# Performance work log

Hardware: AMD Instinct MI355X
Metric: run time of the kernel (lower is better)

The kernel has to match this reference:

```python
import jax, jax.numpy as jnp
import numpy as np

N_NODES = 50000
N_EDGES = 800000
IN_FEATS = 128
H_FEATS = 128
OUT_FEATS = 64
N_HEADS = 4
THRESHOLD = 0.1
COS_EPS = 1e-8   # F.cosine_similarity eps
LN_EPS = 1e-5


def setup_inputs() -> dict:
    key = jax.random.key(0)
    ks = jax.random.split(key, 16)
    D1 = H_FEATS // N_HEADS  # 32
    inp = {
        "feat": jax.random.normal(ks[0], (N_NODES, IN_FEATS), dtype=jnp.float32),
        "src": jax.random.randint(ks[1], (N_EDGES,), 0, N_NODES, dtype=jnp.int32),
        "dst": jax.random.randint(ks[2], (N_EDGES,), 0, N_NODES, dtype=jnp.int32),
        # conv0: in_feats -> n_heads * (h_feats // n_heads)
        "W0": jax.random.normal(ks[3], (IN_FEATS, N_HEADS * D1), dtype=jnp.float32) * (1.0 / np.sqrt(IN_FEATS)),
        "b0": jnp.zeros((N_HEADS * D1,), dtype=jnp.float32),
        # conv1: h_feats -> n_heads * (h_feats // n_heads)
        "W1": jax.random.normal(ks[4], (H_FEATS, N_HEADS * D1), dtype=jnp.float32) * (1.0 / np.sqrt(H_FEATS)),
        "b1": jnp.zeros((N_HEADS * D1,), dtype=jnp.float32),
        # conv2: h_feats -> 1 * out_feats
        "W2": jax.random.normal(ks[5], (H_FEATS, OUT_FEATS), dtype=jnp.float32) * (1.0 / np.sqrt(H_FEATS)),
        "b2": jnp.zeros((OUT_FEATS,), dtype=jnp.float32),
        # LayerNorms used after conv0 and conv1 (lns[1], lns[2])
        "ln1_g": jnp.ones((H_FEATS,), dtype=jnp.float32),
        "ln1_b": jnp.zeros((H_FEATS,), dtype=jnp.float32),
        "ln2_g": jnp.ones((H_FEATS,), dtype=jnp.float32),
        "ln2_b": jnp.zeros((H_FEATS,), dtype=jnp.float32),
    }
    return inp


def _layer_norm(x, g, b):
    mu = jnp.mean(x, axis=-1, keepdims=True)
    var = jnp.mean(jnp.square(x - mu), axis=-1, keepdims=True)
    return (x - mu) * jax.lax.rsqrt(var + LN_EPS) * g + b


def _rgat_conv(x, src, dst, W, b, n_heads, d_out):
    N = x.shape[0]
    ft = (x @ W).reshape(N, n_heads, d_out)  # (N, H, D)
    # edge score: cosine_similarity(src_feat_flat, src_feat_flat) -> per-node, then gather
    flat = ft.reshape(N, n_heads * d_out)
    sq = jnp.sum(flat * flat, axis=1)                      # (N,)
    nrm = jnp.maximum(jnp.sqrt(sq), COS_EPS)
    cos = sq / (nrm * nrm)                                 # ~1 for nonzero rows
    e_node = jnp.log(jnp.where(cos >= THRESHOLD, cos, 1e-6))
    e = e_node[src]                                        # (E,)
    # segment softmax over destination nodes (DGL edge_softmax)
    m = jax.ops.segment_max(e, dst, num_segments=N)
    m = jnp.where(jnp.isfinite(m), m, 0.0)                 # empty segments
    ex = jnp.exp(e - m[dst])
    den = jax.ops.segment_sum(ex, dst, num_segments=N)
    a = ex / jnp.maximum(den[dst], 1e-16)                  # (E,)
    # u_mul_e + sum aggregation
    msg = ft[src] * a[:, None, None]                       # (E, H, D)
    out = jax.ops.segment_sum(msg, dst, num_segments=N)    # (N, H, D)
    return out + b.reshape(1, n_heads, d_out)


def reference(feat, src, dst, W0, b0, W1, b1, W2, b2, ln1_g, ln1_b, ln2_g, ln2_b):
    N = feat.shape[0]
    D1 = H_FEATS // N_HEADS
    x = _rgat_conv(feat, src, dst, W0, b0, N_HEADS, D1).reshape(N, -1)
    x = jax.nn.relu(_layer_norm(x, ln1_g, ln1_b))
    x = _rgat_conv(x, src, dst, W1, b1, N_HEADS, D1).reshape(N, -1)
    x = jax.nn.relu(_layer_norm(x, ln2_g, ln2_b))
    x = _rgat_conv(x, src, dst, W2, b2, 1, OUT_FEATS).reshape(N, -1)
    return x
```

## Files before the change

kernel.cpp:

```cpp
#include <hip/hip_runtime.h>
#include <hip/hip_fp16.h>
#include <math.h>

#define NN 50000
#define NE 800000
#define NB 196
#define CPAD 16
#define STILE 4096
#define BCAP 8192

typedef _Float16 v8h __attribute__((ext_vector_type(8)));
typedef float v4f __attribute__((ext_vector_type(4)));

__global__ __launch_bounds__(256) void convert_kernel(
    const float* __restrict__ W0, const float* __restrict__ W1,
    const float* __restrict__ W2, __half* __restrict__ W0T,
    __half* __restrict__ W1T, __half* __restrict__ W2T,
    int* __restrict__ bhist) {
  int gid = blockIdx.x * 256 + threadIdx.x;
  if (gid < NB * CPAD) bhist[gid] = 0;
  if (gid < 16384) {
    int n = gid >> 7, k = gid & 127;
    W0T[gid] = __float2half(W0[k * 128 + n]);
  } else if (gid < 32768) {
    int g = gid - 16384; int n = g >> 7, k = g & 127;
    W1T[g] = __float2half(W1[k * 128 + n]);
  } else if (gid < 40960) {
    int g = gid - 32768; int n = g >> 7, k = g & 127;
    W2T[g] = __float2half(W2[k * 64 + n]);
  }
}

template <int OUT, bool F32IN>
__global__ __launch_bounds__(256) void gemm_mfma(
    const void* __restrict__ Xv, const __half* __restrict__ WT,
    __half* __restrict__ Y, int nrows) {
  constexpr int NT = OUT / 16;
  __shared__ __align__(16) __half Xs[64][136];
  __shared__ __align__(16) __half Ws[OUT][136];
  const int tid = threadIdx.x;
  const int row0 = blockIdx.x * 64;
#pragma unroll
  for (int i = 0; i < 4; i++) {
    int ci = tid + 256 * i;
    int r = ci >> 4, ch = ci & 15;
    int g = row0 + r;
    if (F32IN) {
      const float* X32 = (const float*)Xv;
      float4 a0 = make_float4(0.f, 0.f, 0.f, 0.f), a1 = a0;
      if (g < nrows) {
        a0 = *(const float4*)&X32[(size_t)g * 128 + ch * 8];
        a1 = *(const float4*)&X32[(size_t)g * 128 + ch * 8 + 4];
      }
      union { __half2 h2[4]; int4 i4; } u;
      u.h2[0] = __floats2half2_rn(a0.x, a0.y);
      u.h2[1] = __floats2half2_rn(a0.z, a0.w);
      u.h2[2] = __floats2half2_rn(a1.x, a1.y);
      u.h2[3] = __floats2half2_rn(a1.z, a1.w);
      *(int4*)&Xs[r][ch * 8] = u.i4;
    } else {
      const __half* X16 = (const __half*)Xv;
      int4 v = make_int4(0, 0, 0, 0);
      if (g < nrows) v = *(const int4*)&X16[(size_t)g * 128 + ch * 8];
      *(int4*)&Xs[r][ch * 8] = v;
    }
  }
#pragma unroll
  for (int i = 0; i < NT; i++) {
    int ci = tid + 256 * i;
    int n = ci >> 4, ch = ci & 15;
    *(int4*)&Ws[n][ch * 8] = *(const int4*)&WT[(size_t)n * 128 + ch * 8];
  }
  __syncthreads();
  const int lane = tid & 63;
  const int w = tid >> 6;
  const int c16 = lane & 15, q = lane >> 4;
  v8h a[4];
#pragma unroll
  for (int kt = 0; kt < 4; kt++)
    a[kt] = *(const v8h*)&Xs[w * 16 + c16][kt * 32 + q * 8];
  v4f acc[NT];
#pragma unroll
  for (int t = 0; t < NT; t++) acc[t] = (v4f){0.f, 0.f, 0.f, 0.f};
#pragma unroll
  for (int t = 0; t < NT; t++) {
#pragma unroll
    for (int kt = 0; kt < 4; kt++) {
      v8h bfr = *(const v8h*)&Ws[t * 16 + c16][kt * 32 + q * 8];
      acc[t] = __builtin_amdgcn_mfma_f32_16x16x32_f16(a[kt], bfr, acc[t], 0, 0, 0);
    }
  }
#pragma unroll
  for (int t = 0; t < NT; t++)
#pragma unroll
    for (int r = 0; r < 4; r++)
      Xs[w * 16 + q * 4 + r][t * 16 + c16] = __float2half(acc[t][r]);
  __syncthreads();
  constexpr int OCH = OUT / 8;
#pragma unroll
  for (int i = 0; i < 64 * OCH / 256; i++) {
    int ci = tid + 256 * i;
    int r = ci / OCH, ch = ci % OCH;
    int g = row0 + r;
    if (g < nrows) *(int4*)&Y[(size_t)g * OUT + ch * 8] = *(const int4*)&Xs[r][ch * 8];
  }
}

template <int F, bool LN, bool HOUT>
__global__ __launch_bounds__(256) void agg_kernel(
    const __half* __restrict__ ft,
    const int* __restrict__ row_ptr, const unsigned short* __restrict__ es,
    const float* __restrict__ bias, const float* __restrict__ g,
    const float* __restrict__ beta, void* __restrict__ out_v, int n) {
  int gw = (blockIdx.x * blockDim.x + threadIdx.x) >> 6;
  int lane = threadIdx.x & 63;
  if (gw >= n) return;
  int b = row_ptr[gw], e = row_ptr[gw + 1];
  int deg = e - b;

  constexpr int LPR = F / 8;
  constexpr int EW  = 64 / LPR;
  const int sub = lane / LPR;
  const int ll  = lane % LPR;
  __half2 hacc[4];
#pragma unroll
  for (int q = 0; q < 4; q++) hacc[q] = __floats2half2_rn(0.f, 0.f);

  for (int cb = b; cb < e; cb += 64) {
    int rem = e - cb; if (rem > 64) rem = 64;
    int sn_l = 0;
    if (lane < rem) sn_l = es[cb + lane];
    for (int j = 0; j < rem; j += EW) {
      int jj = j + sub;
      int sn = __shfl(sn_l, jj, 64);
      if (jj < rem) {
        union { float4 f4; __half2 h2[4]; } u;
        u.f4 = *(const float4*)&ft[(size_t)sn * F + ll * 8];
#pragma unroll
        for (int q = 0; q < 4; q++) hacc[q] = __hadd2(hacc[q], u.h2[q]);
      }
    }
  }

#pragma unroll
  for (int o = 32; o >= LPR; o >>= 1) {
#pragma unroll
    for (int q = 0; q < 4; q++) {
      union { __half2 h; int i; } a, s;
      a.h = hacc[q];
      s.i = __shfl_xor(a.i, o, 64);
      hacc[q] = __hadd2(a.h, s.h);
    }
  }

  float acc[8];
#pragma unroll
  for (int q = 0; q < 4; q++) {
    float2 f = __half22float2(hacc[q]);
    acc[2 * q + 0] = f.x;
    acc[2 * q + 1] = f.y;
  }

  float sc = (deg > 0) ? (1.0f / (float)deg) : 0.f;
  float4 b4a = *(const float4*)&bias[ll * 8 + 0];
  float4 b4b = *(const float4*)&bias[ll * 8 + 4];
  acc[0] = fmaf(acc[0], sc, b4a.x); acc[1] = fmaf(acc[1], sc, b4a.y);
  acc[2] = fmaf(acc[2], sc, b4a.z); acc[3] = fmaf(acc[3], sc, b4a.w);
  acc[4] = fmaf(acc[4], sc, b4b.x); acc[5] = fmaf(acc[5], sc, b4b.y);
  acc[6] = fmaf(acc[6], sc, b4b.z); acc[7] = fmaf(acc[7], sc, b4b.w);

  if (LN) {
    float sum = 0.f;
#pragma unroll
    for (int q = 0; q < 8; q++) sum += acc[q];
#pragma unroll
    for (int o = LPR / 2; o > 0; o >>= 1) sum += __shfl_xor(sum, o, 64);
    float mean = sum * (1.0f / 128.0f);
    float var = 0.f;
#pragma unroll
    for (int q = 0; q < 8; q++) { acc[q] -= mean; var = fmaf(acc[q], acc[q], var); }
#pragma unroll
    for (int o = LPR / 2; o > 0; o >>= 1) var += __shfl_xor(var, o, 64);
    float r = rsqrtf(var * (1.0f / 128.0f) + 1e-5f);
    float4 g4a = *(const float4*)&g[ll * 8 + 0];
    float4 g4b = *(const float4*)&g[ll * 8 + 4];
    float4 be4a = *(const float4*)&beta[ll * 8 + 0];
    float4 be4b = *(const float4*)&beta[ll * 8 + 4];
    acc[0] = fmaxf(acc[0] * r * g4a.x + be4a.x, 0.f);
    acc[1] = fmaxf(acc[1] * r * g4a.y + be4a.y, 0.f);
    acc[2] = fmaxf(acc[2] * r * g4a.z + be4a.z, 0.f);
    acc[3] = fmaxf(acc[3] * r * g4a.w + be4a.w, 0.f);
    acc[4] = fmaxf(acc[4] * r * g4b.x + be4b.x, 0.f);
    acc[5] = fmaxf(acc[5] * r * g4b.y + be4b.y, 0.f);
    acc[6] = fmaxf(acc[6] * r * g4b.z + be4b.z, 0.f);
    acc[7] = fmaxf(acc[7] * r * g4b.w + be4b.w, 0.f);
  }
  if (sub == 0) {
    if (HOUT) {
      __half* outh = (__half*)out_v;
      union { __half2 h2[4]; int4 i4; } u;
      u.h2[0] = __floats2half2_rn(acc[0], acc[1]);
      u.h2[1] = __floats2half2_rn(acc[2], acc[3]);
      u.h2[2] = __floats2half2_rn(acc[4], acc[5]);
      u.h2[3] = __floats2half2_rn(acc[6], acc[7]);
      *(int4*)&outh[(size_t)gw * F + ll * 8] = u.i4;
    } else {
      float* outf = (float*)out_v;
      *(float4*)&outf[(size_t)gw * F + ll * 8 + 0] = make_float4(acc[0], acc[1], acc[2], acc[3]);
      *(float4*)&outf[(size_t)gw * F + ll * 8 + 4] = make_float4(acc[4], acc[5], acc[6], acc[7]);
    }
  }
}

__global__ __launch_bounds__(256) void stage_kernel(const int* __restrict__ src,
                                                    const int* __restrict__ dst,
                                                    int* __restrict__ bhist,
                                                    int* __restrict__ staged) {
  __shared__ int cnt[256];
  __shared__ int basep[256];
  __shared__ int cur[256];
  int tid = threadIdx.x;
  cnt[tid] = 0;
  cur[tid] = 0;
  __syncthreads();
#pragma unroll
  for (int q = 0; q < 4; q++) {
    int base = blockIdx.x * STILE + q * 1024 + tid * 4;
    if (base + 3 < NE) {
      int4 d = *(const int4*)&dst[base];
      atomicAdd(&cnt[d.x >> 8], 1);
      atomicAdd(&cnt[d.y >> 8], 1);
      atomicAdd(&cnt[d.z >> 8], 1);
      atomicAdd(&cnt[d.w >> 8], 1);
    } else {
#pragma unroll
      for (int k = 0; k < 4; k++)
        if (base + k < NE) atomicAdd(&cnt[dst[base + k] >> 8], 1);
    }
  }
  __syncthreads();
  if (tid < NB) basep[tid] = (cnt[tid] > 0) ? atomicAdd(&bhist[tid * CPAD], cnt[tid]) : 0;
  __syncthreads();
#pragma unroll
  for (int q = 0; q < 4; q++) {
    int base = blockIdx.x * STILE + q * 1024 + tid * 4;
    if (base + 3 < NE) {
      int4 d = *(const int4*)&dst[base];
      int4 s = *(const int4*)&src[base];
      int b0 = d.x >> 8, b1 = d.y >> 8, b2 = d.z >> 8, b3 = d.w >> 8;
      int p0 = atomicAdd(&cur[b0], 1);
      staged[b0 * BCAP + basep[b0] + p0] = s.x | ((d.x & 255) << 16);
      int p1 = atomicAdd(&cur[b1], 1);
      staged[b1 * BCAP + basep[b1] + p1] = s.y | ((d.y & 255) << 16);
      int p2 = atomicAdd(&cur[b2], 1);
      staged[b2 * BCAP + basep[b2] + p2] = s.z | ((d.z & 255) << 16);
      int p3 = atomicAdd(&cur[b3], 1);
      staged[b3 * BCAP + basep[b3] + p3] = s.w | ((d.w & 255) << 16);
    } else {
#pragma unroll
      for (int k = 0; k < 4; k++) {
        if (base + k < NE) {
          int d = dst[base + k], s = src[base + k];
          int bb = d >> 8;
          int pp = atomicAdd(&cur[bb], 1);
          staged[bb * BCAP + basep[bb] + pp] = s | ((d & 255) << 16);
        }
      }
    }
  }
}

__global__ __launch_bounds__(256) void bucket_csr_kernel(const int* __restrict__ staged,
                                                         const int* __restrict__ bhist,
                                                         int* __restrict__ row_ptr,
                                                         unsigned short* __restrict__ es) {
  int b = blockIdx.x;
  int tid = threadIdx.x;
  int lane = tid & 63, wid = tid >> 6;
  __shared__ int sbase[256];
  __shared__ int wsum[4];
  __shared__ int cnt[256];
  __shared__ int fill_l[256];
  int tv = (tid < NB) ? bhist[tid * CPAD] : 0;
  int x = tv;
#pragma unroll
  for (int o = 1; o < 64; o <<= 1) {
    int y = __shfl_up(x, o, 64);
    if (lane >= o) x += y;
  }
  if (lane == 63) wsum[wid] = x;
  __syncthreads();
  int wpre = 0;
  for (int w = 0; w < wid; w++) wpre += wsum[w];
  sbase[tid] = wpre + x - tv;
  cnt[tid] = 0;
  __syncthreads();
  int lo = sbase[b];
  int cntb = bhist[b * CPAD];
  const int* st = &staged[b * BCAP];
  for (int i = tid; i < cntb; i += 256)
    atomicAdd(&cnt[(st[i] >> 16) & 255], 1);
  __syncthreads();
  int v = cnt[tid];
  x = v;
#pragma unroll
  for (int o = 1; o < 64; o <<= 1) {
    int y = __shfl_up(x, o, 64);
    if (lane >= o) x += y;
  }
  __syncthreads();
  if (lane == 63) wsum[wid] = x;
  __syncthreads();
  wpre = 0;
  for (int w = 0; w < wid; w++) wpre += wsum[w];
  int start = lo + wpre + x - v;
  int node = (b << 8) + tid;
  if (node < NN) row_ptr[node] = start;
  fill_l[tid] = start;
  __syncthreads();
  for (int i = tid; i < cntb; i += 256) {
    int w = st[i];
    int pos = atomicAdd(&fill_l[(w >> 16) & 255], 1);
    es[pos] = (unsigned short)(w & 0xFFFF);
  }
  if (b == 0 && tid == 0) row_ptr[NN] = NE;
}

extern "C" void kernel_launch(void* const* d_in, const int* in_sizes, int n_in,
                              void* d_out, int out_size, void* d_ws, size_t ws_size,
                              hipStream_t stream) {
  (void)in_sizes; (void)n_in; (void)out_size; (void)ws_size;
  const float* feat = (const float*)d_in[0];
  const int* src = (const int*)d_in[1];
  const int* dst = (const int*)d_in[2];
  const float* W0 = (const float*)d_in[3];
  const float* b0 = (const float*)d_in[4];
  const float* W1 = (const float*)d_in[5];
  const float* b1 = (const float*)d_in[6];
  const float* W2 = (const float*)d_in[7];
  const float* b2 = (const float*)d_in[8];
  const float* ln1g = (const float*)d_in[9];
  const float* ln1b = (const float*)d_in[10];
  const float* ln2g = (const float*)d_in[11];
  const float* ln2b = (const float*)d_in[12];
  float* out = (float*)d_out;

  char* p = (char*)d_ws;
  auto alloc = [&](size_t bytes) {
    char* r = p;
    p += (bytes + 255) & ~size_t(255);
    return r;
  };
  __half* fth      = (__half*)alloc((size_t)NN * 128 * 2);
  __half* hh       = (__half*)alloc((size_t)NN * 128 * 2);
  __half* W0T      = (__half*)alloc(128 * 128 * 2);
  __half* W1T      = (__half*)alloc(128 * 128 * 2);
  __half* W2T      = (__half*)alloc(64 * 128 * 2);
  int* row_ptr     = (int*)alloc((size_t)(NN + 1) * 4);
  unsigned short* es = (unsigned short*)alloc((size_t)NE * 2);
  int* staged      = (int*)alloc((size_t)NB * BCAP * 4);
  int* bhist       = (int*)alloc((size_t)NB * CPAD * 4);

  convert_kernel<<<160, 256, 0, stream>>>(W0, W1, W2, W0T, W1T, W2T, bhist);

  int sb = (NE + STILE - 1) / STILE;
  stage_kernel<<<sb, 256, 0, stream>>>(src, dst, bhist, staged);
  bucket_csr_kernel<<<NB, 256, 0, stream>>>(staged, bhist, row_ptr, es);

  int gb = (NN + 63) / 64;
  int nwb = (NN + 3) / 4;

  gemm_mfma<128, true><<<gb, 256, 0, stream>>>(feat, W0T, fth, NN);
  agg_kernel<128, true, true><<<nwb, 256, 0, stream>>>(fth, row_ptr, es, b0, ln1g, ln1b, hh, NN);
  gemm_mfma<128, false><<<gb, 256, 0, stream>>>(hh, W1T, fth, NN);
  agg_kernel<128, true, true><<<nwb, 256, 0, stream>>>(fth, row_ptr, es, b1, ln2g, ln2b, hh, NN);
  gemm_mfma<64, false><<<gb, 256, 0, stream>>>(hh, W2T, fth, NN);
  agg_kernel<64, false, false><<<nwb, 256, 0, stream>>>(fth, row_ptr, es, b2, nullptr, nullptr, out, NN);
}
```

Baseline: 238.9 us.

## Split aggregation into 32-column chunks and move LayerNorm into next GEMM prologue

The aggregation kernel now launches one wave per node per 32-feature column chunk, using blockIdx.y to select the chunk. Each lane loads two neighbor rows per iteration, which gives more waves and more independent loads in flight for the gather. Because a wave no longer sees a whole row, LayerNorm+ReLU moves out of aggregation and into the next GEMM's input-loading stage, using 16-lane shuffles per row. The cost is that each node's edge list is read several times (once per chunk), and the per-row LN statistics are computed on fp16-rounded aggregates.

```diff
diff --git a/kernel.cpp b/kernel.cpp
--- a/kernel.cpp
+++ b/kernel.cpp
@@ -31,9 +31,10 @@
   }
 }
 
-template <int OUT, bool F32IN>
+template <int OUT, bool F32IN, bool LN>
 __global__ __launch_bounds__(256) void gemm_mfma(
     const void* __restrict__ Xv, const __half* __restrict__ WT,
+    const float* __restrict__ lng, const float* __restrict__ lnb,
     __half* __restrict__ Y, int nrows) {
   constexpr int NT = OUT / 16;
   __shared__ __align__(16) __half Xs[64][136];
@@ -62,7 +63,47 @@
       const __half* X16 = (const __half*)Xv;
       int4 v = make_int4(0, 0, 0, 0);
       if (g < nrows) v = *(const int4*)&X16[(size_t)g * 128 + ch * 8];
-      *(int4*)&Xs[r][ch * 8] = v;
+      if (LN) {
+        union { int4 i4; __half2 h2[4]; } u; u.i4 = v;
+        float x[8];
+#pragma unroll
+        for (int q = 0; q < 4; q++) {
+          float2 f = __half22float2(u.h2[q]);
+          x[2 * q + 0] = f.x; x[2 * q + 1] = f.y;
+        }
+        float s = 0.f;
+#pragma unroll
+        for (int q = 0; q < 8; q++) s += x[q];
+#pragma unroll
+        for (int o = 1; o < 16; o <<= 1) s += __shfl_xor(s, o, 64);
+        float mean = s * (1.0f / 128.0f);
+        float var = 0.f;
+#pragma unroll
+        for (int q = 0; q < 8; q++) { x[q] -= mean; var = fmaf(x[q], x[q], var); }
+#pragma unroll
+        for (int o = 1; o < 16; o <<= 1) var += __shfl_xor(var, o, 64);
+        float rr = rsqrtf(var * (1.0f / 128.0f) + 1e-5f);
+        float4 g4a = *(const float4*)&lng[ch * 8 + 0];
+        float4 g4b = *(const float4*)&lng[ch * 8 + 4];
+        float4 bea = *(const float4*)&lnb[ch * 8 + 0];
+        float4 beb = *(const float4*)&lnb[ch * 8 + 4];
+        x[0] = fmaxf(fmaf(x[0] * rr, g4a.x, bea.x), 0.f);
+        x[1] = fmaxf(fmaf(x[1] * rr, g4a.y, bea.y), 0.f);
+        x[2] = fmaxf(fmaf(x[2] * rr, g4a.z, bea.z), 0.f);
+        x[3] = fmaxf(fmaf(x[3] * rr, g4a.w, bea.w), 0.f);
+        x[4] = fmaxf(fmaf(x[4] * rr, g4b.x, beb.x), 0.f);
+        x[5] = fmaxf(fmaf(x[5] * rr, g4b.y, beb.y), 0.f);
+        x[6] = fmaxf(fmaf(x[6] * rr, g4b.z, beb.z), 0.f);
+        x[7] = fmaxf(fmaf(x[7] * rr, g4b.w, beb.w), 0.f);
+        union { __half2 h2[4]; int4 i4; } w;
+        w.h2[0] = __floats2half2_rn(x[0], x[1]);
+        w.h2[1] = __floats2half2_rn(x[2], x[3]);
+        w.h2[2] = __floats2half2_rn(x[4], x[5]);
+        w.h2[3] = __floats2half2_rn(x[6], x[7]);
+        *(int4*)&Xs[r][ch * 8] = w.i4;
+      } else {
+        *(int4*)&Xs[r][ch * 8] = v;
+      }
     }
   }
 #pragma unroll
@@ -106,44 +147,48 @@
   }
 }
 
-template <int F, bool LN, bool HOUT>
-__global__ __launch_bounds__(256) void agg_kernel(
+template <int F, bool F32OUT>
+__global__ __launch_bounds__(256) void agg_chunk_kernel(
     const __half* __restrict__ ft,
     const int* __restrict__ row_ptr, const unsigned short* __restrict__ es,
-    const float* __restrict__ bias, const float* __restrict__ g,
-    const float* __restrict__ beta, void* __restrict__ out_v, int n) {
-  int gw = (blockIdx.x * blockDim.x + threadIdx.x) >> 6;
+    const float* __restrict__ bias, void* __restrict__ out_v, int n) {
+  int gw = blockIdx.x * 4 + (threadIdx.x >> 6);
   int lane = threadIdx.x & 63;
+  int chk = blockIdx.y;
   if (gw >= n) return;
   int b = row_ptr[gw], e = row_ptr[gw + 1];
   int deg = e - b;
 
-  constexpr int LPR = F / 8;
-  constexpr int EW  = 64 / LPR;
-  const int sub = lane / LPR;
-  const int ll  = lane % LPR;
+  const int sub = lane >> 2;
+  const int ll = lane & 3;
+  const __half* ftc = ft + (size_t)chk * 32 + (size_t)ll * 8;
+
   __half2 hacc[4];
 #pragma unroll
   for (int q = 0; q < 4; q++) hacc[q] = __floats2half2_rn(0.f, 0.f);
 
   for (int cb = b; cb < e; cb += 64) {
     int rem = e - cb; if (rem > 64) rem = 64;
-    int sn_l = 0;
-    if (lane < rem) sn_l = es[cb + lane];
-    for (int j = 0; j < rem; j += EW) {
-      int jj = j + sub;
-      int sn = __shfl(sn_l, jj, 64);
-      if (jj < rem) {
-        union { float4 f4; __half2 h2[4]; } u;
-        u.f4 = *(const float4*)&ft[(size_t)sn * F + ll * 8];
-#pragma unroll
-        for (int q = 0; q < 4; q++) hacc[q] = __hadd2(hacc[q], u.h2[q]);
-      }
-    }
-  }
-
-#pragma unroll
-  for (int o = 32; o >= LPR; o >>= 1) {
+    int sn_l = (lane < rem) ? (int)es[cb + lane] : 0;
+    for (int j = 0; j < rem; j += 32) {
+      int jj0 = j + sub;
+      int jj1 = j + 16 + sub;
+      int sn0 = __shfl(sn_l, jj0, 64);
+      int sn1 = __shfl(sn_l, jj1 & 63, 64);
+      union { float4 f4; __half2 h2[4]; } u0, u1;
+      u0.f4 = make_float4(0.f, 0.f, 0.f, 0.f);
+      u1.f4 = make_float4(0.f, 0.f, 0.f, 0.f);
+      if (jj0 < rem) u0.f4 = *(const float4*)&ftc[(size_t)sn0 * F];
+      if (jj1 < rem) u1.f4 = *(const float4*)&ftc[(size_t)sn1 * F];
+#pragma unroll
+      for (int q = 0; q < 4; q++) hacc[q] = __hadd2(hacc[q], u0.h2[q]);
+#pragma unroll
+      for (int q = 0; q < 4; q++) hacc[q] = __hadd2(hacc[q], u1.h2[q]);
+    }
+  }
+
+#pragma unroll
+  for (int o = 32; o >= 4; o >>= 1) {
 #pragma unroll
     for (int q = 0; q < 4; q++) {
       union { __half2 h; int i; } a, s;
@@ -153,61 +198,35 @@
     }
   }
 
-  float acc[8];
-#pragma unroll
-  for (int q = 0; q < 4; q++) {
-    float2 f = __half22float2(hacc[q]);
-    acc[2 * q + 0] = f.x;
-    acc[2 * q + 1] = f.y;
-  }
-
-  float sc = (deg > 0) ? (1.0f / (float)deg) : 0.f;
-  float4 b4a = *(const float4*)&bias[ll * 8 + 0];
-  float4 b4b = *(const float4*)&bias[ll * 8 + 4];
-  acc[0] = fmaf(acc[0], sc, b4a.x); acc[1] = fmaf(acc[1], sc, b4a.y);
-  acc[2] = fmaf(acc[2], sc, b4a.z); acc[3] = fmaf(acc[3], sc, b4a.w);
-  acc[4] = fmaf(acc[4], sc, b4b.x); acc[5] = fmaf(acc[5], sc, b4b.y);
-  acc[6] = fmaf(acc[6], sc, b4b.z); acc[7] = fmaf(acc[7], sc, b4b.w);
-
-  if (LN) {
-    float sum = 0.f;
-#pragma unroll
-    for (int q = 0; q < 8; q++) sum += acc[q];
-#pragma unroll
-    for (int o = LPR / 2; o > 0; o >>= 1) sum += __shfl_xor(sum, o, 64);
-    float mean = sum * (1.0f / 128.0f);
-    float var = 0.f;
-#pragma unroll
-    for (int q = 0; q < 8; q++) { acc[q] -= mean; var = fmaf(acc[q], acc[q], var); }
-#pragma unroll
-    for (int o = LPR / 2; o > 0; o >>= 1) var += __shfl_xor(var, o, 64);
-    float r = rsqrtf(var * (1.0f / 128.0f) + 1e-5f);
-    float4 g4a = *(const float4*)&g[ll * 8 + 0];
-    float4 g4b = *(const float4*)&g[ll * 8 + 4];
-    float4 be4a = *(const float4*)&beta[ll * 8 + 0];
-    float4 be4b = *(const float4*)&beta[ll * 8 + 4];
-    acc[0] = fmaxf(acc[0] * r * g4a.x + be4a.x, 0.f);
-    acc[1] = fmaxf(acc[1] * r * g4a.y + be4a.y, 0.f);
-    acc[2] = fmaxf(acc[2] * r * g4a.z + be4a.z, 0.f);
-    acc[3] = fmaxf(acc[3] * r * g4a.w + be4a.w, 0.f);
-    acc[4] = fmaxf(acc[4] * r * g4b.x + be4b.x, 0.f);
-    acc[5] = fmaxf(acc[5] * r * g4b.y + be4b.y, 0.f);
-    acc[6] = fmaxf(acc[6] * r * g4b.z + be4b.z, 0.f);
-    acc[7] = fmaxf(acc[7] * r * g4b.w + be4b.w, 0.f);
-  }
   if (sub == 0) {
-    if (HOUT) {
+    float acc[8];
+#pragma unroll
+    for (int q = 0; q < 4; q++) {
+      float2 f = __half22float2(hacc[q]);
+      acc[2 * q + 0] = f.x;
+      acc[2 * q + 1] = f.y;
+    }
+    float sc = (deg > 0) ? (1.0f / (float)deg) : 0.f;
+    float4 b4a = *(const float4*)&bias[chk * 32 + ll * 8 + 0];
+    float4 b4b = *(const float4*)&bias[chk * 32 + ll * 8 + 4];
+    acc[0] = fmaf(acc[0], sc, b4a.x); acc[1] = fmaf(acc[1], sc, b4a.y);
+    acc[2] = fmaf(acc[2], sc, b4a.z); acc[3] = fmaf(acc[3], sc, b4a.w);
+    acc[4] = fmaf(acc[4], sc, b4b.x); acc[5] = fmaf(acc[5], sc, b4b.y);
+    acc[6] = fmaf(acc[6], sc, b4b.z); acc[7] = fmaf(acc[7], sc, b4b.w);
+    if (F32OUT) {
+      float* outf = (float*)out_v;
+      *(float4*)&outf[(size_t)gw * F + chk * 32 + ll * 8 + 0] =
+          make_float4(acc[0], acc[1], acc[2], acc[3]);
+      *(float4*)&outf[(size_t)gw * F + chk * 32 + ll * 8 + 4] =
+          make_float4(acc[4], acc[5], acc[6], acc[7]);
+    } else {
       __half* outh = (__half*)out_v;
       union { __half2 h2[4]; int4 i4; } u;
       u.h2[0] = __floats2half2_rn(acc[0], acc[1]);
       u.h2[1] = __floats2half2_rn(acc[2], acc[3]);
       u.h2[2] = __floats2half2_rn(acc[4], acc[5]);
       u.h2[3] = __floats2half2_rn(acc[6], acc[7]);
-      *(int4*)&outh[(size_t)gw * F + ll * 8] = u.i4;
-    } else {
-      float* outf = (float*)out_v;
-      *(float4*)&outf[(size_t)gw * F + ll * 8 + 0] = make_float4(acc[0], acc[1], acc[2], acc[3]);
-      *(float4*)&outf[(size_t)gw * F + ll * 8 + 4] = make_float4(acc[4], acc[5], acc[6], acc[7]);
+      *(int4*)&outh[(size_t)gw * F + chk * 32 + ll * 8] = u.i4;
     }
   }
 }
@@ -368,12 +387,12 @@
   bucket_csr_kernel<<<NB, 256, 0, stream>>>(staged, bhist, row_ptr, es);
 
   int gb = (NN + 63) / 64;
-  int nwb = (NN + 3) / 4;
-
-  gemm_mfma<128, true><<<gb, 256, 0, stream>>>(feat, W0T, fth, NN);
-  agg_kernel<128, true, true><<<nwb, 256, 0, stream>>>(fth, row_ptr, es, b0, ln1g, ln1b, hh, NN);
-  gemm_mfma<128, false><<<gb, 256, 0, stream>>>(hh, W1T, fth, NN);
-  agg_kernel<128, true, true><<<nwb, 256, 0, stream>>>(fth, row_ptr, es, b1, ln2g, ln2b, hh, NN);
-  gemm_mfma<64, false><<<gb, 256, 0, stream>>>(hh, W2T, fth, NN);
-  agg_kernel<64, false, false><<<nwb, 256, 0, stream>>>(fth, row_ptr, es, b2, nullptr, nullptr, out, NN);
-}
+  int ab = (NN + 3) / 4;
+
+  gemm_mfma<128, true, false><<<gb, 256, 0, stream>>>(feat, W0T, nullptr, nullptr, fth, NN);
+  agg_chunk_kernel<128, false><<<dim3(ab, 4), 256, 0, stream>>>(fth, row_ptr, es, b0, hh, NN);
+  gemm_mfma<128, false, true><<<gb, 256, 0, stream>>>(hh, W1T, ln1g, ln1b, fth, NN);
+  agg_chunk_kernel<128, false><<<dim3(ab, 4), 256, 0, stream>>>(fth, row_ptr, es, b1, hh, NN);
+  gemm_mfma<64, false, true><<<gb, 256, 0, stream>>>(hh, W2T, ln2g, ln2b, fth, NN);
+  agg_chunk_kernel<64, true><<<dim3(ab, 2), 256, 0, stream>>>(fth, row_ptr, es, b2, out, NN);
+}
```

After: 302.1 us. 26.5% more time.

## Fuse CSR bucket build with first GEMM and pipeline gather loads in aggregation

Applied to the files above, without the earlier changes.

The layer-0 GEMM now runs in the same launch as the bucket CSR construction: extra blocks do the fp32-to-fp16 matmul while the first NB blocks build row_ptr and the edge list, with shared memory held in a union. Edge entries become ints holding a precomputed byte offset (node<<8), so the gather needs no multiply, though the edge list doubles in size. The aggregation loop issues DEPTH independent 16-byte gathers per iteration before accumulating, which raises memory-level parallelism. One launch goes away and the two independent phases overlap. The cost is a larger edge list and more live registers in the aggregation kernel.

```diff
diff --git a/kernel.cpp b/kernel.cpp
--- a/kernel.cpp
+++ b/kernel.cpp
@@ -8,6 +8,7 @@
 #define CPAD 16
 #define STILE 4096
 #define BCAP 8192
+#define GB0 782
 
 typedef _Float16 v8h __attribute__((ext_vector_type(8)));
 typedef float v4f __attribute__((ext_vector_type(4)));
@@ -31,187 +32,6 @@
   }
 }
 
-template <int OUT, bool F32IN>
-__global__ __launch_bounds__(256) void gemm_mfma(
-    const void* __restrict__ Xv, const __half* __restrict__ WT,
-    __half* __restrict__ Y, int nrows) {
-  constexpr int NT = OUT / 16;
-  __shared__ __align__(16) __half Xs[64][136];
-  __shared__ __align__(16) __half Ws[OUT][136];
-  const int tid = threadIdx.x;
-  const int row0 = blockIdx.x * 64;
-#pragma unroll
-  for (int i = 0; i < 4; i++) {
-    int ci = tid + 256 * i;
-    int r = ci >> 4, ch = ci & 15;
-    int g = row0 + r;
-    if (F32IN) {
-      const float* X32 = (const float*)Xv;
-      float4 a0 = make_float4(0.f, 0.f, 0.f, 0.f), a1 = a0;
-      if (g < nrows) {
-        a0 = *(const float4*)&X32[(size_t)g * 128 + ch * 8];
-        a1 = *(const float4*)&X32[(size_t)g * 128 + ch * 8 + 4];
-      }
-      union { __half2 h2[4]; int4 i4; } u;
-      u.h2[0] = __floats2half2_rn(a0.x, a0.y);
-      u.h2[1] = __floats2half2_rn(a0.z, a0.w);
-      u.h2[2] = __floats2half2_rn(a1.x, a1.y);
-      u.h2[3] = __floats2half2_rn(a1.z, a1.w);
-      *(int4*)&Xs[r][ch * 8] = u.i4;
-    } else {
-      const __half* X16 = (const __half*)Xv;
-      int4 v = make_int4(0, 0, 0, 0);
-      if (g < nrows) v = *(const int4*)&X16[(size_t)g * 128 + ch * 8];
-      *(int4*)&Xs[r][ch * 8] = v;
-    }
-  }
-#pragma unroll
-  for (int i = 0; i < NT; i++) {
-    int ci = tid + 256 * i;
-    int n = ci >> 4, ch = ci & 15;
-    *(int4*)&Ws[n][ch * 8] = *(const int4*)&WT[(size_t)n * 128 + ch * 8];
-  }
-  __syncthreads();
-  const int lane = tid & 63;
-  const int w = tid >> 6;
-  const int c16 = lane & 15, q = lane >> 4;
-  v8h a[4];
-#pragma unroll
-  for (int kt = 0; kt < 4; kt++)
-    a[kt] = *(const v8h*)&Xs[w * 16 + c16][kt * 32 + q * 8];
-  v4f acc[NT];
-#pragma unroll
-  for (int t = 0; t < NT; t++) acc[t] = (v4f){0.f, 0.f, 0.f, 0.f};
-#pragma unroll
-  for (int t = 0; t < NT; t++) {
-#pragma unroll
-    for (int kt = 0; kt < 4; kt++) {
-      v8h bfr = *(const v8h*)&Ws[t * 16 + c16][kt * 32 + q * 8];
-      acc[t] = __builtin_amdgcn_mfma_f32_16x16x32_f16(a[kt], bfr, acc[t], 0, 0, 0);
-    }
-  }
-#pragma unroll
-  for (int t = 0; t < NT; t++)
-#pragma unroll
-    for (int r = 0; r < 4; r++)
-      Xs[w * 16 + q * 4 + r][t * 16 + c16] = __float2half(acc[t][r]);
-  __syncthreads();
-  constexpr int OCH = OUT / 8;
-#pragma unroll
-  for (int i = 0; i < 64 * OCH / 256; i++) {
-    int ci = tid + 256 * i;
-    int r = ci / OCH, ch = ci % OCH;
-    int g = row0 + r;
-    if (g < nrows) *(int4*)&Y[(size_t)g * OUT + ch * 8] = *(const int4*)&Xs[r][ch * 8];
-  }
-}
-
-template <int F, bool LN, bool HOUT>
-__global__ __launch_bounds__(256) void agg_kernel(
-    const __half* __restrict__ ft,
-    const int* __restrict__ row_ptr, const unsigned short* __restrict__ es,
-    const float* __restrict__ bias, const float* __restrict__ g,
-    const float* __restrict__ beta, void* __restrict__ out_v, int n) {
-  int gw = (blockIdx.x * blockDim.x + threadIdx.x) >> 6;
-  int lane = threadIdx.x & 63;
-  if (gw >= n) return;
-  int b = row_ptr[gw], e = row_ptr[gw + 1];
-  int deg = e - b;
-
-  constexpr int LPR = F / 8;
-  constexpr int EW  = 64 / LPR;
-  const int sub = lane / LPR;
-  const int ll  = lane % LPR;
-  __half2 hacc[4];
-#pragma unroll
-  for (int q = 0; q < 4; q++) hacc[q] = __floats2half2_rn(0.f, 0.f);
-
-  for (int cb = b; cb < e; cb += 64) {
-    int rem = e - cb; if (rem > 64) rem = 64;
-    int sn_l = 0;
-    if (lane < rem) sn_l = es[cb + lane];
-    for (int j = 0; j < rem; j += EW) {
-      int jj = j + sub;
-      int sn = __shfl(sn_l, jj, 64);
-      if (jj < rem) {
-        union { float4 f4; __half2 h2[4]; } u;
-        u.f4 = *(const float4*)&ft[(size_t)sn * F + ll * 8];
-#pragma unroll
-        for (int q = 0; q < 4; q++) hacc[q] = __hadd2(hacc[q], u.h2[q]);
-      }
-    }
-  }
-
-#pragma unroll
-  for (int o = 32; o >= LPR; o >>= 1) {
-#pragma unroll
-    for (int q = 0; q < 4; q++) {
-      union { __half2 h; int i; } a, s;
-      a.h = hacc[q];
-      s.i = __shfl_xor(a.i, o, 64);
-      hacc[q] = __hadd2(a.h, s.h);
-    }
-  }
-
-  float acc[8];
-#pragma unroll
-  for (int q = 0; q < 4; q++) {
-    float2 f = __half22float2(hacc[q]);
-    acc[2 * q + 0] = f.x;
-    acc[2 * q + 1] = f.y;
-  }
-
-  float sc = (deg > 0) ? (1.0f / (float)deg) : 0.f;
-  float4 b4a = *(const float4*)&bias[ll * 8 + 0];
-  float4 b4b = *(const float4*)&bias[ll * 8 + 4];
-  acc[0] = fmaf(acc[0], sc, b4a.x); acc[1] = fmaf(acc[1], sc, b4a.y);
-  acc[2] = fmaf(acc[2], sc, b4a.z); acc[3] = fmaf(acc[3], sc, b4a.w);
-  acc[4] = fmaf(acc[4], sc, b4b.x); acc[5] = fmaf(acc[5], sc, b4b.y);
-  acc[6] = fmaf(acc[6], sc, b4b.z); acc[7] = fmaf(acc[7], sc, b4b.w);
-
-  if (LN) {
-    float sum = 0.f;
-#pragma unroll
-    for (int q = 0; q < 8; q++) sum += acc[q];
-#pragma unroll
-    for (int o = LPR / 2; o > 0; o >>= 1) sum += __shfl_xor(sum, o, 64);
-    float mean = sum * (1.0f / 128.0f);
-    float var = 0.f;
-#pragma unroll
-    for (int q = 0; q < 8; q++) { acc[q] -= mean; var = fmaf(acc[q], acc[q], var); }
-#pragma unroll
-    for (int o = LPR / 2; o > 0; o >>= 1) var += __shfl_xor(var, o, 64);
-    float r = rsqrtf(var * (1.0f / 128.0f) + 1e-5f);
-    float4 g4a = *(const float4*)&g[ll * 8 + 0];
-    float4 g4b = *(const float4*)&g[ll * 8 + 4];
-    float4 be4a = *(const float4*)&beta[ll * 8 + 0];
-    float4 be4b = *(const float4*)&beta[ll * 8 + 4];
-    acc[0] = fmaxf(acc[0] * r * g4a.x + be4a.x, 0.f);
-    acc[1] = fmaxf(acc[1] * r * g4a.y + be4a.y, 0.f);
-    acc[2] = fmaxf(acc[2] * r * g4a.z + be4a.z, 0.f);
-    acc[3] = fmaxf(acc[3] * r * g4a.w + be4a.w, 0.f);
-    acc[4] = fmaxf(acc[4] * r * g4b.x + be4b.x, 0.f);
-    acc[5] = fmaxf(acc[5] * r * g4b.y + be4b.y, 0.f);
-    acc[6] = fmaxf(acc[6] * r * g4b.z + be4b.z, 0.f);
-    acc[7] = fmaxf(acc[7] * r * g4b.w + be4b.w, 0.f);
-  }
-  if (sub == 0) {
-    if (HOUT) {
-      __half* outh = (__half*)out_v;
-      union { __half2 h2[4]; int4 i4; } u;
-      u.h2[0] = __floats2half2_rn(acc[0], acc[1]);
-      u.h2[1] = __floats2half2_rn(acc[2], acc[3]);
-      u.h2[2] = __floats2half2_rn(acc[4], acc[5]);
-      u.h2[3] = __floats2half2_rn(acc[6], acc[7]);
-      *(int4*)&outh[(size_t)gw * F + ll * 8] = u.i4;
-    } else {
-      float* outf = (float*)out_v;
-      *(float4*)&outf[(size_t)gw * F + ll * 8 + 0] = make_float4(acc[0], acc[1], acc[2], acc[3]);
-      *(float4*)&outf[(size_t)gw * F + ll * 8 + 4] = make_float4(acc[4], acc[5], acc[6], acc[7]);
-    }
-  }
-}
-
 __global__ __launch_bounds__(256) void stage_kernel(const int* __restrict__ src,
                                                     const int* __restrict__ dst,
                                                     int* __restrict__ bhist,
@@ -270,17 +90,79 @@
   }
 }
 
-__global__ __launch_bounds__(256) void bucket_csr_kernel(const int* __restrict__ staged,
-                                                         const int* __restrict__ bhist,
-                                                         int* __restrict__ row_ptr,
-                                                         unsigned short* __restrict__ es) {
+__global__ __launch_bounds__(256) void bucket_gemm0_fused(
+    const int* __restrict__ staged, const int* __restrict__ bhist,
+    int* __restrict__ row_ptr, int* __restrict__ es,
+    const float* __restrict__ feat, const __half* __restrict__ W0T,
+    __half* __restrict__ Y) {
+  __shared__ __align__(16) union {
+    struct { __half Xs[64][136]; __half Ws[128][136]; } g;
+    struct { int sbase[256]; int wsum[4]; int cnt[256]; int fill_l[256]; } c;
+  } sh;
+  const int tid = threadIdx.x;
+
+  if (blockIdx.x >= NB) {
+    const int row0 = (blockIdx.x - NB) * 64;
+#pragma unroll
+    for (int i = 0; i < 4; i++) {
+      int ci = tid + 256 * i;
+      int r = ci >> 4, ch = ci & 15;
+      int g = row0 + r;
+      float4 a0 = make_float4(0.f, 0.f, 0.f, 0.f), a1 = a0;
+      if (g < NN) {
+        a0 = *(const float4*)&feat[(size_t)g * 128 + ch * 8];
+        a1 = *(const float4*)&feat[(size_t)g * 128 + ch * 8 + 4];
+      }
+      union { __half2 h2[4]; int4 i4; } u;
+      u.h2[0] = __floats2half2_rn(a0.x, a0.y);
+      u.h2[1] = __floats2half2_rn(a0.z, a0.w);
+      u.h2[2] = __floats2half2_rn(a1.x, a1.y);
+      u.h2[3] = __floats2half2_rn(a1.z, a1.w);
+      *(int4*)&sh.g.Xs[r][ch * 8] = u.i4;
+    }
+#pragma unroll
+    for (int i = 0; i < 8; i++) {
+      int ci = tid + 256 * i;
+      int n = ci >> 4, ch = ci & 15;
+      *(int4*)&sh.g.Ws[n][ch * 8] = *(const int4*)&W0T[(size_t)n * 128 + ch * 8];
+    }
+    __syncthreads();
+    const int lane = tid & 63;
+    const int w = tid >> 6;
+    const int c16 = lane & 15, q = lane >> 4;
+    v8h a[4];
+#pragma unroll
+    for (int kt = 0; kt < 4; kt++)
+      a[kt] = *(const v8h*)&sh.g.Xs[w * 16 + c16][kt * 32 + q * 8];
+    v4f acc[8];
+#pragma unroll
+    for (int t = 0; t < 8; t++) acc[t] = (v4f){0.f, 0.f, 0.f, 0.f};
+#pragma unroll
+    for (int t = 0; t < 8; t++) {
+#pragma unroll
+      for (int kt = 0; kt < 4; kt++) {
+        v8h bfr = *(const v8h*)&sh.g.Ws[t * 16 + c16][kt * 32 + q * 8];
+        acc[t] = __builtin_amdgcn_mfma_f32_16x16x32_f16(a[kt], bfr, acc[t], 0, 0, 0);
+      }
+    }
+#pragma unroll
+    for (int t = 0; t < 8; t++)
+#pragma unroll
+      for (int r = 0; r < 4; r++)
+        sh.g.Xs[w * 16 + q * 4 + r][t * 16 + c16] = __float2half(acc[t][r]);
+    __syncthreads();
+#pragma unroll
+    for (int i = 0; i < 4; i++) {
+      int ci = tid + 256 * i;
+      int r = ci / 16, ch = ci % 16;
+      int g = row0 + r;
+      if (g < NN) *(int4*)&Y[(size_t)g * 128 + ch * 8] = *(const int4*)&sh.g.Xs[r][ch * 8];
+    }
+    return;
+  }
+
   int b = blockIdx.x;
-  int tid = threadIdx.x;
   int lane = tid & 63, wid = tid >> 6;
-  __shared__ int sbase[256];
-  __shared__ int wsum[4];
-  __shared__ int cnt[256];
-  __shared__ int fill_l[256];
   int tv = (tid < NB) ? bhist[tid * CPAD] : 0;
   int x = tv;
 #pragma unroll
@@ -288,20 +170,20 @@
     int y = __shfl_up(x, o, 64);
     if (lane >= o) x += y;
   }
-  if (lane == 63) wsum[wid] = x;
+  if (lane == 63) sh.c.wsum[wid] = x;
   __syncthreads();
   int wpre = 0;
-  for (int w = 0; w < wid; w++) wpre += wsum[w];
-  sbase[tid] = wpre + x - tv;
-  cnt[tid] = 0;
-  __syncthreads();
-  int lo = sbase[b];
+  for (int w = 0; w < wid; w++) wpre += sh.c.wsum[w];
+  sh.c.sbase[tid] = wpre + x - tv;
+  sh.c.cnt[tid] = 0;
+  __syncthreads();
+  int lo = sh.c.sbase[b];
   int cntb = bhist[b * CPAD];
   const int* st = &staged[b * BCAP];
   for (int i = tid; i < cntb; i += 256)
-    atomicAdd(&cnt[(st[i] >> 16) & 255], 1);
-  __syncthreads();
-  int v = cnt[tid];
+    atomicAdd(&sh.c.cnt[(st[i] >> 16) & 255], 1);
+  __syncthreads();
+  int v = sh.c.cnt[tid];
   x = v;
 #pragma unroll
   for (int o = 1; o < 64; o <<= 1) {
@@ -309,21 +191,217 @@
     if (lane >= o) x += y;
   }
   __syncthreads();
-  if (lane == 63) wsum[wid] = x;
+  if (lane == 63) sh.c.wsum[wid] = x;
   __syncthreads();
   wpre = 0;
-  for (int w = 0; w < wid; w++) wpre += wsum[w];
+  for (int w = 0; w < wid; w++) wpre += sh.c.wsum[w];
   int start = lo + wpre + x - v;
   int node = (b << 8) + tid;
   if (node < NN) row_ptr[node] = start;
-  fill_l[tid] = start;
+  sh.c.fill_l[tid] = start;
   __syncthreads();
   for (int i = tid; i < cntb; i += 256) {
     int w = st[i];
-    int pos = atomicAdd(&fill_l[(w >> 16) & 255], 1);
-    es[pos] = (unsigned short)(w & 0xFFFF);
+    int pos = atomicAdd(&sh.c.fill_l[(w >> 16) & 255], 1);
+    es[pos] = (w & 0xFFFF) << 8;
   }
   if (b == 0 && tid == 0) row_ptr[NN] = NE;
+}
+
+template <int OUT>
+__global__ __launch_bounds__(256) void gemm_mfma(
+    const __half* __restrict__ X16, const __half* __restrict__ WT,
+    __half* __restrict__ Y, int nrows) {
+  constexpr int NT = OUT / 16;
+  __shared__ __align__(16) __half Xs[64][136];
+  __shared__ __align__(16) __half Ws[OUT][136];
+  const int tid = threadIdx.x;
+  const int row0 = blockIdx.x * 64;
+#pragma unroll
+  for (int i = 0; i < 4; i++) {
+    int ci = tid + 256 * i;
+    int r = ci >> 4, ch = ci & 15;
+    int g = row0 + r;
+    int4 v = make_int4(0, 0, 0, 0);
+    if (g < nrows) v = *(const int4*)&X16[(size_t)g * 128 + ch * 8];
+    *(int4*)&Xs[r][ch * 8] = v;
+  }
+#pragma unroll
+  for (int i = 0; i < NT; i++) {
+    int ci = tid + 256 * i;
+    int n = ci >> 4, ch = ci & 15;
+    *(int4*)&Ws[n][ch * 8] = *(const int4*)&WT[(size_t)n * 128 + ch * 8];
+  }
+  __syncthreads();
+  const int lane = tid & 63;
+  const int w = tid >> 6;
+  const int c16 = lane & 15, q = lane >> 4;
+  v8h a[4];
+#pragma unroll
+  for (int kt = 0; kt < 4; kt++)
+    a[kt] = *(const v8h*)&Xs[w * 16 + c16][kt * 32 + q * 8];
+  v4f acc[NT];
+#pragma unroll
+  for (int t = 0; t < NT; t++) acc[t] = (v4f){0.f, 0.f, 0.f, 0.f};
+#pragma unroll
+  for (int t = 0; t < NT; t++) {
+#pragma unroll
+    for (int kt = 0; kt < 4; kt++) {
+      v8h bfr = *(const v8h*)&Ws[t * 16 + c16][kt * 32 + q * 8];
+      acc[t] = __builtin_amdgcn_mfma_f32_16x16x32_f16(a[kt], bfr, acc[t], 0, 0, 0);
+    }
+  }
+#pragma unroll
+  for (int t = 0; t < NT; t++)
+#pragma unroll
+    for (int r = 0; r < 4; r++)
+      Xs[w * 16 + q * 4 + r][t * 16 + c16] = __float2half(acc[t][r]);
+  __syncthreads();
+  constexpr int OCH = OUT / 8;
+#pragma unroll
+  for (int i = 0; i < 64 * OCH / 256; i++) {
+    int ci = tid + 256 * i;
+    int r = ci / OCH, ch = ci % OCH;
+    int g = row0 + r;
+    if (g < nrows) *(int4*)&Y[(size_t)g * OUT + ch * 8] = *(const int4*)&Xs[r][ch * 8];
+  }
+}
+
+template <int F, bool LN, bool HOUT>
+__global__ __launch_bounds__(256) void agg_kernel(
+    const __half* __restrict__ ft,
+    const int* __restrict__ row_ptr, const int* __restrict__ es,
+    const float* __restrict__ bias, const float* __restrict__ g,
+    const float* __restrict__ beta, void* __restrict__ out_v, int n) {
+  int gw = (blockIdx.x * blockDim.x + threadIdx.x) >> 6;
+  int lane = threadIdx.x & 63;
+  if (gw >= n) return;
+  int b = row_ptr[gw], e = row_ptr[gw + 1];
+  int deg = e - b;
+
+  constexpr int LPR = F / 8;
+  constexpr int EW  = 64 / LPR;
+  constexpr int DEPTH = (F == 128) ? 4 : 2;
+  constexpr int GRP = DEPTH * EW;
+  const int sub = lane / LPR;
+  const int ll  = lane % LPR;
+  const int ll16 = ll * 16;
+  const char* ftb = (const char*)ft;
+  __half2 hacc[4];
+#pragma unroll
+  for (int q = 0; q < 4; q++) hacc[q] = __floats2half2_rn(0.f, 0.f);
+
+  for (int cb = b; cb < e; cb += 64) {
+    int rem = e - cb; if (rem > 64) rem = 64;
+    int sn_l = 0;
+    if (lane < rem) sn_l = es[cb + lane];
+    int nfull = rem & ~(GRP - 1);
+    for (int j = 0; j < nfull; j += GRP) {
+      int o[DEPTH];
+#pragma unroll
+      for (int d = 0; d < DEPTH; d++) {
+        o[d] = __shfl(sn_l, j + d * EW + sub, 64);
+        if (F == 64) o[d] >>= 1;
+      }
+      union { float4 f4; __half2 h2[4]; } u[DEPTH];
+#pragma unroll
+      for (int d = 0; d < DEPTH; d++)
+        u[d].f4 = *(const float4*)(ftb + (unsigned)(o[d] + ll16));
+#pragma unroll
+      for (int d = 0; d < DEPTH; d++)
+#pragma unroll
+        for (int q = 0; q < 4; q++) hacc[q] = __hadd2(hacc[q], u[d].h2[q]);
+    }
+    if (nfull < rem) {
+      int j = nfull;
+      int jj[DEPTH], o[DEPTH];
+#pragma unroll
+      for (int d = 0; d < DEPTH; d++) {
+        jj[d] = j + d * EW + sub;
+        o[d] = __shfl(sn_l, jj[d] & 63, 64);
+        if (F == 64) o[d] >>= 1;
+      }
+      union { float4 f4; __half2 h2[4]; } u[DEPTH];
+#pragma unroll
+      for (int d = 0; d < DEPTH; d++) {
+        u[d].f4 = make_float4(0.f, 0.f, 0.f, 0.f);
+        if (jj[d] < rem) u[d].f4 = *(const float4*)(ftb + (unsigned)(o[d] + ll16));
+      }
+#pragma unroll
+      for (int d = 0; d < DEPTH; d++)
+#pragma unroll
+        for (int q = 0; q < 4; q++) hacc[q] = __hadd2(hacc[q], u[d].h2[q]);
+    }
+  }
+
+#pragma unroll
+  for (int o = 32; o >= LPR; o >>= 1) {
+#pragma unroll
+    for (int q = 0; q < 4; q++) {
+      union { __half2 h; int i; } a, s;
+      a.h = hacc[q];
+      s.i = __shfl_xor(a.i, o, 64);
+      hacc[q] = __hadd2(a.h, s.h);
+    }
+  }
+
+  float acc[8];
+#pragma unroll
+  for (int q = 0; q < 4; q++) {
+    float2 f = __half22float2(hacc[q]);
+    acc[2 * q + 0] = f.x;
+    acc[2 * q + 1] = f.y;
+  }
+
+  float sc = (deg > 0) ? (1.0f / (float)deg) : 0.f;
+  float4 b4a = *(const float4*)&bias[ll * 8 + 0];
+  float4 b4b = *(const float4*)&bias[ll * 8 + 4];
+  acc[0] = fmaf(acc[0], sc, b4a.x); acc[1] = fmaf(acc[1], sc, b4a.y);
+  acc[2] = fmaf(acc[2], sc, b4a.z); acc[3] = fmaf(acc[3], sc, b4a.w);
+  acc[4] = fmaf(acc[4], sc, b4b.x); acc[5] = fmaf(acc[5], sc, b4b.y);
+  acc[6] = fmaf(acc[6], sc, b4b.z); acc[7] = fmaf(acc[7], sc, b4b.w);
+
+  if (LN) {
+    float sum = 0.f;
+#pragma unroll
+    for (int q = 0; q < 8; q++) sum += acc[q];
+#pragma unroll
+    for (int o = LPR / 2; o > 0; o >>= 1) sum += __shfl_xor(sum, o, 64);
+    float mean = sum * (1.0f / 128.0f);
+    float var = 0.f;
+#pragma unroll
+    for (int q = 0; q < 8; q++) { acc[q] -= mean; var = fmaf(acc[q], acc[q], var); }
+#pragma unroll
+    for (int o = LPR / 2; o > 0; o >>= 1) var += __shfl_xor(var, o, 64);
+    float r = rsqrtf(var * (1.0f / 128.0f) + 1e-5f);
+    float4 g4a = *(const float4*)&g[ll * 8 + 0];
+    float4 g4b = *(const float4*)&g[ll * 8 + 4];
+    float4 be4a = *(const float4*)&beta[ll * 8 + 0];
+    float4 be4b = *(const float4*)&beta[ll * 8 + 4];
+    acc[0] = fmaxf(acc[0] * r * g4a.x + be4a.x, 0.f);
+    acc[1] = fmaxf(acc[1] * r * g4a.y + be4a.y, 0.f);
+    acc[2] = fmaxf(acc[2] * r * g4a.z + be4a.z, 0.f);
+    acc[3] = fmaxf(acc[3] * r * g4a.w + be4a.w, 0.f);
+    acc[4] = fmaxf(acc[4] * r * g4b.x + be4b.x, 0.f);
+    acc[5] = fmaxf(acc[5] * r * g4b.y + be4b.y, 0.f);
+    acc[6] = fmaxf(acc[6] * r * g4b.z + be4b.z, 0.f);
+    acc[7] = fmaxf(acc[7] * r * g4b.w + be4b.w, 0.f);
+  }
+  if (sub == 0) {
+    if (HOUT) {
+      __half* outh = (__half*)out_v;
+      union { __half2 h2[4]; int4 i4; } u;
+      u.h2[0] = __floats2half2_rn(acc[0], acc[1]);
+      u.h2[1] = __floats2half2_rn(acc[2], acc[3]);
+      u.h2[2] = __floats2half2_rn(acc[4], acc[5]);
+      u.h2[3] = __floats2half2_rn(acc[6], acc[7]);
+      *(int4*)&outh[(size_t)gw * F + ll * 8] = u.i4;
+    } else {
+      float* outf = (float*)out_v;
+      *(float4*)&outf[(size_t)gw * F + ll * 8 + 0] = make_float4(acc[0], acc[1], acc[2], acc[3]);
+      *(float4*)&outf[(size_t)gw * F + ll * 8 + 4] = make_float4(acc[4], acc[5], acc[6], acc[7]);
+    }
+  }
 }
 
 extern "C" void kernel_launch(void* const* d_in, const int* in_sizes, int n_in,
@@ -357,7 +435,7 @@
   __half* W1T      = (__half*)alloc(128 * 128 * 2);
   __half* W2T      = (__half*)alloc(64 * 128 * 2);
   int* row_ptr     = (int*)alloc((size_t)(NN + 1) * 4);
-  unsigned short* es = (unsigned short*)alloc((size_t)NE * 2);
+  int* es          = (int*)alloc((size_t)NE * 4);
   int* staged      = (int*)alloc((size_t)NB * BCAP * 4);
   int* bhist       = (int*)alloc((size_t)NB * CPAD * 4);
 
@@ -365,15 +443,15 @@
 
   int sb = (NE + STILE - 1) / STILE;
   stage_kernel<<<sb, 256, 0, stream>>>(src, dst, bhist, staged);
-  bucket_csr_kernel<<<NB, 256, 0, stream>>>(staged, bhist, row_ptr, es);
+
+  bucket_gemm0_fused<<<NB + GB0, 256, 0, stream>>>(staged, bhist, row_ptr, es, feat, W0T, fth);
 
   int gb = (NN + 63) / 64;
   int nwb = (NN + 3) / 4;
 
-  gemm_mfma<128, true><<<gb, 256, 0, stream>>>(feat, W0T, fth, NN);
   agg_kernel<128, true, true><<<nwb, 256, 0, stream>>>(fth, row_ptr, es, b0, ln1g, ln1b, hh, NN);
-  gemm_mfma<128, false><<<gb, 256, 0, stream>>>(hh, W1T, fth, NN);
+  gemm_mfma<128><<<gb, 256, 0, stream>>>(hh, W1T, fth, NN);
   agg_kernel<128, true, true><<<nwb, 256, 0, stream>>>(fth, row_ptr, es, b1, ln2g, ln2b, hh, NN);
-  gemm_mfma<64, false><<<gb, 256, 0, stream>>>(hh, W2T, fth, NN);
+  gemm_mfma<64><<<gb, 256, 0, stream>>>(hh, W2T, fth, NN);
   agg_kernel<64, false, false><<<nwb, 256, 0, stream>>>(fth, row_ptr, es, b2, nullptr, nullptr, out, NN);
 }
```

Result: faster. 216.4 us (-9.4%).
